# Kernel tuning notes

Measured on AMD Instinct MI355X. Metric: run time of the kernel, lower is better.

Reference implementation:

```python
import jax, jax.numpy as jnp
import numpy as np

B, T, E, H = 8, 1024, 1024, 16
D = E // H  # head_dim = 64
MAX_OFFSET = 0.5


def setup_inputs() -> dict:
    key = jax.random.key(0)
    ks = jax.random.split(key, 12)
    s = 0.02
    return {
        "query": jax.random.normal(ks[0], (B, T, E), jnp.float32),
        "key_": jax.random.normal(ks[1], (B, T, E), jnp.float32),
        "value": jax.random.normal(ks[2], (B, T, E), jnp.float32),
        "Wq": jax.random.normal(ks[3], (E, E), jnp.float32) * s,
        "bq": jnp.zeros((E,), jnp.float32),
        "Wk": jax.random.normal(ks[4], (E, E), jnp.float32) * s,
        "bk": jnp.zeros((E,), jnp.float32),
        "Wv": jax.random.normal(ks[5], (E, E), jnp.float32) * s,
        "bv": jnp.zeros((E,), jnp.float32),
        "Wo": jax.random.normal(ks[6], (E, E), jnp.float32) * s,
        "bo": jnp.zeros((E,), jnp.float32),
        "bias_table": jax.random.normal(ks[7], (2 * T - 1, H), jnp.float32) * s,
        "offset": jax.random.normal(ks[8], (1,), jnp.float32) * 0.1,
    }


def _temporal_bias(bias_table, offset):
    # relative position index: [T, T] in [0, 2T-2]
    coords = jnp.arange(T)
    rel = (coords[:, None] - coords[None, :]) + (T - 1)
    bounded = jnp.tanh(offset) * MAX_OFFSET  # scalar (shape (1,))
    adj = jnp.clip(rel.astype(jnp.float32) + bounded, 0.0, 2.0 * T - 2.0)
    lo = jnp.floor(adj).astype(jnp.int32)
    hi = jnp.ceil(adj).astype(jnp.int32)
    w = adj - lo.astype(jnp.float32)  # [T, T]
    lo_val = bias_table[lo]  # [T, T, H]
    hi_val = bias_table[hi]  # [T, T, H]
    bias = lo_val * (1.0 - w[..., None]) + hi_val * w[..., None]
    # -> [1, H, T, T]
    return jnp.transpose(bias, (2, 0, 1))[None]


def reference(query, key_, value, Wq, bq, Wk, bk, Wv, bv, Wo, bo, bias_table, offset):
    scale = D ** -0.5
    # torch Linear: x @ W.T + b
    q = (jnp.einsum('bte,fe->btf', query, Wq) + bq).reshape(B, T, H, D).transpose(0, 2, 1, 3)
    k = (jnp.einsum('bte,fe->btf', key_, Wk) + bk).reshape(B, T, H, D).transpose(0, 2, 1, 3)
    v = (jnp.einsum('bte,fe->btf', value, Wv) + bv).reshape(B, T, H, D).transpose(0, 2, 1, 3)
    scores = jnp.einsum('bhqd,bhkd->bhqk', q, k) * scale  # [B, H, T, T]
    scores = scores + _temporal_bias(bias_table, offset)
    attn = jax.nn.softmax(scores, axis=-1)
    out = jnp.einsum('bhqk,bhkd->bhqd', attn, v)  # [B, H, T, D]
    out = out.transpose(0, 2, 1, 3).reshape(B, T, E)
    return jnp.einsum('bte,fe->btf', out, Wo) + bo
```

## Files before the change

### kernel.cpp

```cpp
#include <hip/hip_runtime.h>
#include <hip/hip_bf16.h>
#include <stdint.h>

#define B_ 8
#define T_ 1024
#define E_ 1024
#define H_ 16
#define D_ 64
#define NREL 2047

using bf16 = __hip_bfloat16;
typedef __attribute__((ext_vector_type(8))) short bhalf8;
typedef __attribute__((ext_vector_type(4))) float f32x4;

typedef __attribute__((address_space(3))) uint32_t lds32_t;
typedef const __attribute__((address_space(1))) uint32_t glb32_t;
__device__ __forceinline__ void gld_lds16(const bf16* g, bf16* l) {
  __builtin_amdgcn_global_load_lds((glb32_t*)(const void*)g, (lds32_t*)(void*)l, 16, 0, 0);
}

__global__ __launch_bounds__(256) void cvt_f32_bf16(const float* __restrict__ s,
                                                    bf16* __restrict__ d, int n) {
  const int i = (blockIdx.x * 256 + threadIdx.x) * 8;
  if (i >= n) return;
  const float4 a = *(const float4*)(s + i);
  const float4 b = *(const float4*)(s + i + 4);
  bf16 t[8];
  t[0] = __float2bfloat16(a.x); t[1] = __float2bfloat16(a.y);
  t[2] = __float2bfloat16(a.z); t[3] = __float2bfloat16(a.w);
  t[4] = __float2bfloat16(b.x); t[5] = __float2bfloat16(b.y);
  t[6] = __float2bfloat16(b.z); t[7] = __float2bfloat16(b.w);
  *(bhalf8*)(d + i) = *(const bhalf8*)t;
}

__global__ void bias_pre(const float* __restrict__ table, const float* __restrict__ offset,
                         float* __restrict__ db) {
  const int idx = blockIdx.x * 256 + threadIdx.x;
  if (idx >= NREL * H_) return;
  const int r = idx >> 4;
  const int h = idx & 15;
  const float bounded = tanhf(offset[0]) * 0.5f;
  float adj = (float)r + bounded;
  adj = fminf(fmaxf(adj, 0.f), 2046.f);
  const int lo = (int)floorf(adj);
  const int hi = (int)ceilf(adj);
  const float wgt = adj - (float)lo;
  const float v = table[lo * H_ + h] * (1.f - wgt) + table[hi * H_ + h] * wgt;
  db[h * NREL + r] = v;
}

template <int SCATTER, int F32OUT>
__global__ __launch_bounds__(256) void gemm_bt(const bf16* __restrict__ A,
                                               const bf16* __restrict__ W,
                                               const float* __restrict__ bias,
                                               void* __restrict__ dst_) {
  __shared__ bf16 As[128 * 32];
  __shared__ bf16 Bs[128 * 32];
  const int tid = threadIdx.x;
  const int lane = tid & 63;
  const int w = tid >> 6;
  const int quad = lane >> 4;
  const int l15 = lane & 15;
  const int m0 = blockIdx.x * 128;
  const int n0 = blockIdx.y * 128;
  const int wm = (w >> 1) * 64;
  const int wn = (w & 1) * 64;

  const f32x4 zero4 = {0.f, 0.f, 0.f, 0.f};
  f32x4 acc[4][4];
#pragma unroll
  for (int i = 0; i < 4; ++i)
#pragma unroll
    for (int j = 0; j < 4; ++j) acc[i][j] = zero4;

  const int srow0 = w * 32 + (lane >> 2);
  const int scol = (lane & 3) * 8;
  const bf16* Ag = A + (size_t)(m0 + srow0) * E_ + scol;
  const bf16* Wg = W + (size_t)(n0 + srow0) * E_ + scol;
  bf16* As0 = As + w * 1024 + lane * 8;
  bf16* Bs0 = Bs + w * 1024 + lane * 8;

  for (int kt = 0; kt < 32; ++kt) {
    __syncthreads();
    const int kc = kt * 32;
    gld_lds16(Ag + kc, As0);
    gld_lds16(Ag + (size_t)16 * E_ + kc, As0 + 512);
    gld_lds16(Wg + kc, Bs0);
    gld_lds16(Wg + (size_t)16 * E_ + kc, Bs0 + 512);
    __syncthreads();

    bhalf8 af[4], bfr[4];
#pragma unroll
    for (int t = 0; t < 4; ++t) {
      af[t] = *(const bhalf8*)(As + (wm + t * 16 + l15) * 32 + quad * 8);
      bfr[t] = *(const bhalf8*)(Bs + (wn + t * 16 + l15) * 32 + quad * 8);
    }
#pragma unroll
    for (int mt = 0; mt < 4; ++mt)
#pragma unroll
      for (int nt = 0; nt < 4; ++nt)
        acc[mt][nt] = __builtin_amdgcn_mfma_f32_16x16x32_bf16(af[mt], bfr[nt], acc[mt][nt], 0, 0, 0);
  }

#pragma unroll
  for (int mt = 0; mt < 4; ++mt) {
#pragma unroll
    for (int nt = 0; nt < 4; ++nt) {
      const int n = n0 + wn + nt * 16 + l15;
      const float bv = bias[n];
#pragma unroll
      for (int r = 0; r < 4; ++r) {
        const int m = m0 + wm + mt * 16 + quad * 4 + r;
        const float v = acc[mt][nt][r] + bv;
        if (SCATTER) {
          const int bb = m >> 10, t = m & 1023, hh = n >> 6, d = n & 63;
          ((bf16*)dst_)[(((size_t)bb * H_ + hh) * T_ + t) * D_ + d] = __float2bfloat16(v);
        } else if (F32OUT) {
          ((float*)dst_)[(size_t)m * E_ + n] = v;
        } else {
          ((bf16*)dst_)[(size_t)m * E_ + n] = __float2bfloat16(v);
        }
      }
    }
  }
}

__global__ __launch_bounds__(256) void attn_kernel(const bf16* __restrict__ Q,
                                                   const bf16* __restrict__ K,
                                                   const bf16* __restrict__ V,
                                                   const float* __restrict__ db,
                                                   bf16* __restrict__ xout) {
  const int tid = threadIdx.x;
  const int lane = tid & 63;
  const int w = tid >> 6;
  const int quad = lane >> 4;
  const int l15 = lane & 15;
  const int bh = blockIdx.x;
  const int h = bh & 15;
  const int b = bh >> 4;
  const int q0 = blockIdx.y * 128;

  __shared__ bf16 Ks[64][72];
  __shared__ bf16 Vt[64][72];
  __shared__ bf16 Ps[4][32][72];
  __shared__ float dbs[1152];

  const size_t base = (size_t)bh * T_ * D_;
  const bf16* Qp = Q + base;
  const bf16* Kp = K + base;
  const bf16* Vp = V + base;
  const float* dbh = db + h * NREL;

  for (int t = tid; t < 1151; t += 256) dbs[t] = dbh[q0 + t];

  const int qw = q0 + w * 32;
  bhalf8 aq[2][2];
#pragma unroll
  for (int mt = 0; mt < 2; ++mt)
#pragma unroll
    for (int ks = 0; ks < 2; ++ks)
      aq[mt][ks] = *(const bhalf8*)(Qp + (size_t)(qw + mt * 16 + l15) * D_ + ks * 32 + quad * 8);

  const f32x4 zero4 = {0.f, 0.f, 0.f, 0.f};
  f32x4 o[2][4];
  float mrow[2][4], lrow[2][4];
#pragma unroll
  for (int mt = 0; mt < 2; ++mt)
#pragma unroll
    for (int nt = 0; nt < 4; ++nt) {
      o[mt][nt] = zero4;
      mrow[mt][nt] = -1e30f;
      lrow[mt][nt] = 0.f;
    }

  for (int it = 0; it < 16; ++it) {
    const int kb = it * 64;
    __syncthreads();
#pragma unroll
    for (int s = 0; s < 2; ++s) {
      const int idx = tid + s * 256;
      const int row = idx >> 3;
      const int c8 = (idx & 7) * 8;
      *(bhalf8*)&Ks[row][c8] = *(const bhalf8*)(Kp + (size_t)(kb + row) * D_ + c8);
      bhalf8 vv = *(const bhalf8*)(Vp + (size_t)(kb + row) * D_ + c8);
      const bf16* vp = (const bf16*)&vv;
      const int kvp = (row + c8) & 63;
#pragma unroll
      for (int j = 0; j < 8; ++j) Vt[c8 + j][kvp] = vp[j];
    }
    __syncthreads();

    f32x4 s4[2][4];
#pragma unroll
    for (int nt = 0; nt < 4; ++nt) {
      const bhalf8 bk0 = *(const bhalf8*)&Ks[nt * 16 + l15][quad * 8];
      const bhalf8 bk1 = *(const bhalf8*)&Ks[nt * 16 + l15][32 + quad * 8];
#pragma unroll
      for (int mt = 0; mt < 2; ++mt) {
        f32x4 a = zero4;
        a = __builtin_amdgcn_mfma_f32_16x16x32_bf16(aq[mt][0], bk0, a, 0, 0, 0);
        a = __builtin_amdgcn_mfma_f32_16x16x32_bf16(aq[mt][1], bk1, a, 0, 0, 0);
        s4[mt][nt] = a;
      }
    }

#pragma unroll
    for (int mt = 0; mt < 2; ++mt) {
#pragma unroll
      for (int r = 0; r < 4; ++r) {
        const int ql = w * 32 + mt * 16 + quad * 4 + r;
        const int ib = ql - kb + 1023;
        float mx = -1e30f;
#pragma unroll
        for (int nt = 0; nt < 4; ++nt) {
          const float sv = s4[mt][nt][r] * 0.125f + dbs[ib - nt * 16 - l15];
          s4[mt][nt][r] = sv;
          mx = fmaxf(mx, sv);
        }
        mx = fmaxf(mx, __shfl_xor(mx, 1, 64));
        mx = fmaxf(mx, __shfl_xor(mx, 2, 64));
        mx = fmaxf(mx, __shfl_xor(mx, 4, 64));
        mx = fmaxf(mx, __shfl_xor(mx, 8, 64));
        const float mnew = fmaxf(mrow[mt][r], mx);
        float sum = 0.f;
#pragma unroll
        for (int nt = 0; nt < 4; ++nt) {
          const float p = __expf(s4[mt][nt][r] - mnew);
          s4[mt][nt][r] = p;
          sum += p;
        }
        sum += __shfl_xor(sum, 1, 64);
        sum += __shfl_xor(sum, 2, 64);
        sum += __shfl_xor(sum, 4, 64);
        sum += __shfl_xor(sum, 8, 64);
        const float alpha = __expf(mrow[mt][r] - mnew);
        lrow[mt][r] = lrow[mt][r] * alpha + sum;
        mrow[mt][r] = mnew;
#pragma unroll
        for (int nt = 0; nt < 4; ++nt) o[mt][nt][r] *= alpha;
      }
    }

#pragma unroll
    for (int mt = 0; mt < 2; ++mt)
#pragma unroll
      for (int nt = 0; nt < 4; ++nt)
#pragma unroll
        for (int r = 0; r < 4; ++r)
          Ps[w][mt * 16 + quad * 4 + r][nt * 16 + l15] = __float2bfloat16(s4[mt][nt][r]);

    bhalf8 pa[2][2];
#pragma unroll
    for (int mt = 0; mt < 2; ++mt)
#pragma unroll
      for (int ks = 0; ks < 2; ++ks)
        pa[mt][ks] = *(const bhalf8*)&Ps[w][mt * 16 + l15][ks * 32 + quad * 8];
    const int rot = (l15 >> 3);
#pragma unroll
    for (int nt = 0; nt < 4; ++nt) {
      const int drow = nt * 16 + l15;
#pragma unroll
      for (int ks = 0; ks < 2; ++ks) {
        const int gp = (4 * ks + quad + 2 * nt + rot) & 7;
        const bhalf8 vb = *(const bhalf8*)&Vt[drow][gp * 8];
#pragma unroll
        for (int mt = 0; mt < 2; ++mt)
          o[mt][nt] = __builtin_amdgcn_mfma_f32_16x16x32_bf16(pa[mt][ks], vb, o[mt][nt], 0, 0, 0);
      }
    }
  }

#pragma unroll
  for (int mt = 0; mt < 2; ++mt) {
#pragma unroll
    for (int nt = 0; nt < 4; ++nt) {
#pragma unroll
      for (int r = 0; r < 4; ++r) {
        const int qrow = qw + mt * 16 + quad * 4 + r;
        xout[((size_t)b * T_ + qrow) * E_ + h * D_ + nt * 16 + l15] =
            __float2bfloat16(o[mt][nt][r] / lrow[mt][r]);
      }
    }
  }
}

extern "C" void kernel_launch(void* const* d_in, const int* in_sizes, int n_in,
                              void* d_out, int out_size, void* d_ws, size_t ws_size,
                              hipStream_t stream) {
  const float* query = (const float*)d_in[0];
  const float* key_  = (const float*)d_in[1];
  const float* value = (const float*)d_in[2];
  const float* Wq = (const float*)d_in[3];
  const float* bq = (const float*)d_in[4];
  const float* Wk = (const float*)d_in[5];
  const float* bk = (const float*)d_in[6];
  const float* Wv = (const float*)d_in[7];
  const float* bv = (const float*)d_in[8];
  const float* Wo = (const float*)d_in[9];
  const float* bo = (const float*)d_in[10];
  const float* table = (const float*)d_in[11];
  const float* offset = (const float*)d_in[12];
  float* out = (float*)d_out;

  char* ws = (char*)d_ws;
  const size_t ME = (size_t)B_ * T_ * E_;
  const size_t EE = (size_t)E_ * E_;
  float* db = (float*)ws;
  bf16* xc  = (bf16*)(ws + 131072);
  bf16* wc  = xc + ME;
  bf16* qb  = wc + 4 * EE;
  bf16* kb  = qb + ME;
  bf16* vb2 = kb + ME;
  bf16* x2  = vb2 + ME;

  dim3 bb(256, 1, 1);
  dim3 gg(64, 8, 1);
  const int gME = (int)(ME / 8 / 256);
  const int gEE = (int)(EE / 8 / 256);

  bias_pre<<<dim3(128), bb, 0, stream>>>(table, offset, db);

  cvt_f32_bf16<<<dim3(gEE), bb, 0, stream>>>(Wq, wc + 0 * EE, (int)EE);
  cvt_f32_bf16<<<dim3(gEE), bb, 0, stream>>>(Wk, wc + 1 * EE, (int)EE);
  cvt_f32_bf16<<<dim3(gEE), bb, 0, stream>>>(Wv, wc + 2 * EE, (int)EE);
  cvt_f32_bf16<<<dim3(gEE), bb, 0, stream>>>(Wo, wc + 3 * EE, (int)EE);

  cvt_f32_bf16<<<dim3(gME), bb, 0, stream>>>(query, xc, (int)ME);
  gemm_bt<1, 0><<<gg, bb, 0, stream>>>(xc, wc + 0 * EE, bq, qb);
  cvt_f32_bf16<<<dim3(gME), bb, 0, stream>>>(key_, xc, (int)ME);
  gemm_bt<1, 0><<<gg, bb, 0, stream>>>(xc, wc + 1 * EE, bk, kb);
  cvt_f32_bf16<<<dim3(gME), bb, 0, stream>>>(value, xc, (int)ME);
  gemm_bt<1, 0><<<gg, bb, 0, stream>>>(xc, wc + 2 * EE, bv, vb2);

  attn_kernel<<<dim3(128, 8, 1), bb, 0, stream>>>(qb, kb, vb2, db, x2);

  gemm_bt<0, 1><<<gg, bb, 0, stream>>>(x2, wc + 3 * EE, bo, out);
}
```

Before: 400.9 us.

## Transpose attention MFMA layout, lazy softmax rescale, direct K loads

Swaps the MFMA operand order so each lane owns one query row, which turns the softmax reductions into cross-quad shuffles and cuts per-row max/sum state from four registers to one. Adds a lazy rescale that only updates the running max when some row's new max exceeds the old one by more than 8. Drops the K shared-memory staging in favour of direct global loads into registers, packs P and output stores as 8-byte vectors, pads Ps, adds setprio around the MFMA sections and sets the launch-bounds occupancy hint. The lazy threshold keeps exponentials bounded by e^8, but K is now re-read from global memory by every wave instead of once per block.

Result: faster. 381.8 us (-4.8%).

```diff
diff --git a/kernel.cpp b/kernel.cpp
--- a/kernel.cpp
+++ b/kernel.cpp
@@ -125,11 +125,11 @@
   }
 }
 
-__global__ __launch_bounds__(256) void attn_kernel(const bf16* __restrict__ Q,
-                                                   const bf16* __restrict__ K,
-                                                   const bf16* __restrict__ V,
-                                                   const float* __restrict__ db,
-                                                   bf16* __restrict__ xout) {
+__global__ __launch_bounds__(256, 4) void attn_kernel(const bf16* __restrict__ Q,
+                                                      const bf16* __restrict__ K,
+                                                      const bf16* __restrict__ V,
+                                                      const float* __restrict__ db,
+                                                      bf16* __restrict__ xout) {
   const int tid = threadIdx.x;
   const int lane = tid & 63;
   const int w = tid >> 6;
@@ -140,9 +140,8 @@
   const int b = bh >> 4;
   const int q0 = blockIdx.y * 128;
 
-  __shared__ bf16 Ks[64][72];
   __shared__ bf16 Vt[64][72];
-  __shared__ bf16 Ps[4][32][72];
+  __shared__ bf16 Ps[4][32][80];
   __shared__ float dbs[1152];
 
   const size_t base = (size_t)bh * T_ * D_;
@@ -163,15 +162,12 @@
 
   const f32x4 zero4 = {0.f, 0.f, 0.f, 0.f};
   f32x4 o[2][4];
-  float mrow[2][4], lrow[2][4];
 #pragma unroll
   for (int mt = 0; mt < 2; ++mt)
 #pragma unroll
-    for (int nt = 0; nt < 4; ++nt) {
-      o[mt][nt] = zero4;
-      mrow[mt][nt] = -1e30f;
-      lrow[mt][nt] = 0.f;
-    }
+    for (int nt = 0; nt < 4; ++nt) o[mt][nt] = zero4;
+  float mrow[2] = {-1e30f, -1e30f};
+  float lrow[2] = {0.f, 0.f};
 
   for (int it = 0; it < 16; ++it) {
     const int kb = it * 64;
@@ -181,7 +177,6 @@
       const int idx = tid + s * 256;
       const int row = idx >> 3;
       const int c8 = (idx & 7) * 8;
-      *(bhalf8*)&Ks[row][c8] = *(const bhalf8*)(Kp + (size_t)(kb + row) * D_ + c8);
       bhalf8 vv = *(const bhalf8*)(Vp + (size_t)(kb + row) * D_ + c8);
       const bf16* vp = (const bf16*)&vv;
       const int kvp = (row + c8) & 63;
@@ -191,71 +186,77 @@
     __syncthreads();
 
     f32x4 s4[2][4];
+    __builtin_amdgcn_s_setprio(1);
 #pragma unroll
     for (int nt = 0; nt < 4; ++nt) {
-      const bhalf8 bk0 = *(const bhalf8*)&Ks[nt * 16 + l15][quad * 8];
-      const bhalf8 bk1 = *(const bhalf8*)&Ks[nt * 16 + l15][32 + quad * 8];
+      const bf16* kr = Kp + (size_t)(kb + nt * 16 + l15) * D_ + quad * 8;
+      const bhalf8 bk0 = *(const bhalf8*)kr;
+      const bhalf8 bk1 = *(const bhalf8*)(kr + 32);
 #pragma unroll
       for (int mt = 0; mt < 2; ++mt) {
         f32x4 a = zero4;
-        a = __builtin_amdgcn_mfma_f32_16x16x32_bf16(aq[mt][0], bk0, a, 0, 0, 0);
-        a = __builtin_amdgcn_mfma_f32_16x16x32_bf16(aq[mt][1], bk1, a, 0, 0, 0);
+        a = __builtin_amdgcn_mfma_f32_16x16x32_bf16(bk0, aq[mt][0], a, 0, 0, 0);
+        a = __builtin_amdgcn_mfma_f32_16x16x32_bf16(bk1, aq[mt][1], a, 0, 0, 0);
         s4[mt][nt] = a;
       }
     }
+    __builtin_amdgcn_s_setprio(0);
 
 #pragma unroll
     for (int mt = 0; mt < 2; ++mt) {
-#pragma unroll
-      for (int r = 0; r < 4; ++r) {
-        const int ql = w * 32 + mt * 16 + quad * 4 + r;
-        const int ib = ql - kb + 1023;
-        float mx = -1e30f;
-#pragma unroll
-        for (int nt = 0; nt < 4; ++nt) {
-          const float sv = s4[mt][nt][r] * 0.125f + dbs[ib - nt * 16 - l15];
+      const int ib = w * 32 + mt * 16 + l15 + 1023 - kb;
+      float tmx = -1e30f;
+#pragma unroll
+      for (int nt = 0; nt < 4; ++nt) {
+#pragma unroll
+        for (int r = 0; r < 4; ++r) {
+          const float sv = s4[mt][nt][r] * 0.125f + dbs[ib - nt * 16 - quad * 4 - r];
           s4[mt][nt][r] = sv;
-          mx = fmaxf(mx, sv);
+          tmx = fmaxf(tmx, sv);
         }
-        mx = fmaxf(mx, __shfl_xor(mx, 1, 64));
-        mx = fmaxf(mx, __shfl_xor(mx, 2, 64));
-        mx = fmaxf(mx, __shfl_xor(mx, 4, 64));
-        mx = fmaxf(mx, __shfl_xor(mx, 8, 64));
-        const float mnew = fmaxf(mrow[mt][r], mx);
-        float sum = 0.f;
-#pragma unroll
-        for (int nt = 0; nt < 4; ++nt) {
-          const float p = __expf(s4[mt][nt][r] - mnew);
+      }
+      tmx = fmaxf(tmx, __shfl_xor(tmx, 16, 64));
+      tmx = fmaxf(tmx, __shfl_xor(tmx, 32, 64));
+      if (!__all(tmx - mrow[mt] <= 8.0f)) {
+        const float mnew = fmaxf(mrow[mt], tmx);
+        const float alpha = __expf(mrow[mt] - mnew);
+        mrow[mt] = mnew;
+        lrow[mt] *= alpha;
+#pragma unroll
+        for (int nt = 0; nt < 4; ++nt) o[mt][nt] *= alpha;
+      }
+      const float mcur = mrow[mt];
+      float sum = 0.f;
+#pragma unroll
+      for (int nt = 0; nt < 4; ++nt) {
+#pragma unroll
+        for (int r = 0; r < 4; ++r) {
+          const float p = __expf(s4[mt][nt][r] - mcur);
           s4[mt][nt][r] = p;
           sum += p;
         }
-        sum += __shfl_xor(sum, 1, 64);
-        sum += __shfl_xor(sum, 2, 64);
-        sum += __shfl_xor(sum, 4, 64);
-        sum += __shfl_xor(sum, 8, 64);
-        const float alpha = __expf(mrow[mt][r] - mnew);
-        lrow[mt][r] = lrow[mt][r] * alpha + sum;
-        mrow[mt][r] = mnew;
-#pragma unroll
-        for (int nt = 0; nt < 4; ++nt) o[mt][nt][r] *= alpha;
-      }
-    }
-
+      }
+      sum += __shfl_xor(sum, 16, 64);
+      sum += __shfl_xor(sum, 32, 64);
+      lrow[mt] += sum;
+
+#pragma unroll
+      for (int nt = 0; nt < 4; ++nt) {
+        alignas(8) bf16 t4[4];
+#pragma unroll
+        for (int r = 0; r < 4; ++r) t4[r] = __float2bfloat16(s4[mt][nt][r]);
+        *(uint2*)&Ps[w][mt * 16 + l15][nt * 16 + quad * 4] = *(const uint2*)t4;
+      }
+    }
+
+    bhalf8 pb[2][2];
 #pragma unroll
     for (int mt = 0; mt < 2; ++mt)
 #pragma unroll
-      for (int nt = 0; nt < 4; ++nt)
-#pragma unroll
-        for (int r = 0; r < 4; ++r)
-          Ps[w][mt * 16 + quad * 4 + r][nt * 16 + l15] = __float2bfloat16(s4[mt][nt][r]);
-
-    bhalf8 pa[2][2];
-#pragma unroll
-    for (int mt = 0; mt < 2; ++mt)
-#pragma unroll
       for (int ks = 0; ks < 2; ++ks)
-        pa[mt][ks] = *(const bhalf8*)&Ps[w][mt * 16 + l15][ks * 32 + quad * 8];
+        pb[mt][ks] = *(const bhalf8*)&Ps[w][mt * 16 + l15][ks * 32 + quad * 8];
     const int rot = (l15 >> 3);
+    __builtin_amdgcn_s_setprio(1);
 #pragma unroll
     for (int nt = 0; nt < 4; ++nt) {
       const int drow = nt * 16 + l15;
@@ -265,21 +266,22 @@
         const bhalf8 vb = *(const bhalf8*)&Vt[drow][gp * 8];
 #pragma unroll
         for (int mt = 0; mt < 2; ++mt)
-          o[mt][nt] = __builtin_amdgcn_mfma_f32_16x16x32_bf16(pa[mt][ks], vb, o[mt][nt], 0, 0, 0);
-      }
-    }
+          o[mt][nt] = __builtin_amdgcn_mfma_f32_16x16x32_bf16(vb, pb[mt][ks], o[mt][nt], 0, 0, 0);
+      }
+    }
+    __builtin_amdgcn_s_setprio(0);
   }
 
 #pragma unroll
   for (int mt = 0; mt < 2; ++mt) {
+    const float inv = 1.f / lrow[mt];
+    const int q = qw + mt * 16 + l15;
 #pragma unroll
     for (int nt = 0; nt < 4; ++nt) {
-#pragma unroll
-      for (int r = 0; r < 4; ++r) {
-        const int qrow = qw + mt * 16 + quad * 4 + r;
-        xout[((size_t)b * T_ + qrow) * E_ + h * D_ + nt * 16 + l15] =
-            __float2bfloat16(o[mt][nt][r] / lrow[mt][r]);
-      }
+      alignas(8) bf16 t4[4];
+#pragma unroll
+      for (int r = 0; r < 4; ++r) t4[r] = __float2bfloat16(o[mt][nt][r] * inv);
+      *(uint2*)&xout[((size_t)b * T_ + q) * E_ + h * D_ + nt * 16 + quad * 4] = *(const uint2*)t4;
     }
   }
 }
```
